# Kernel optimization log

Hardware: AMD Instinct MI355X
Metric: run time of the kernel (lower is better)

## Reference

```python
import jax, jax.numpy as jnp
import numpy as np
from math import sqrt

B, S, D_MODEL = 2, 2048, 1024
H = 16
ADIM = D_MODEL // H  # 64
K_REL = 16
N_PEMB = 2 * K_REL + 1  # 33, bidirectional rel-pos vocabulary


def setup_inputs() -> dict:
    key = jax.random.key(0)
    ks = jax.random.split(key, 8)
    sc = 0.02
    return {
        "iQ": jax.random.normal(ks[0], (B, S, D_MODEL), jnp.float32),
        "iK": jax.random.normal(ks[1], (B, S, D_MODEL), jnp.float32),
        "iV": jax.random.normal(ks[2], (B, S, D_MODEL), jnp.float32),
        "Wq": jax.random.normal(ks[3], (D_MODEL, D_MODEL), jnp.float32) * sc,
        "Wk": jax.random.normal(ks[4], (D_MODEL, D_MODEL), jnp.float32) * sc,
        "Wv": jax.random.normal(ks[5], (D_MODEL, D_MODEL), jnp.float32) * sc,
        "Wo": jax.random.normal(ks[6], (D_MODEL, D_MODEL), jnp.float32) * sc,
        "rel_pemb": jax.random.normal(ks[7], (N_PEMB, ADIM), jnp.float32) * sc,
    }


def reference(iQ, iK, iV, Wq, Wk, Wv, Wo, rel_pemb):
    b, nq, _ = iQ.shape
    seql = iK.shape[1]
    # projections -> [b, h, len, d]
    q = (iQ @ Wq).reshape(b, nq, H, ADIM).transpose(0, 2, 1, 3)
    k = (iK @ Wk).reshape(b, seql, H, ADIM).transpose(0, 2, 1, 3)
    v = (iV @ Wv).reshape(b, seql, H, ADIM).transpose(0, 2, 1, 3)
    # content scores: [b, h, nq, seql]
    scores = jnp.einsum("bhqd,bhsd->bhqs", q, k)
    # relative position bias: rel[i, j] = clamp(j - i, -K, K) + K
    pos = jnp.arange(seql)
    rel = jnp.clip(pos[None, :] - pos[:, None], -K_REL, K_REL) + K_REL
    rel = rel[seql - nq:, :]  # narrow to query rows: [nq, seql]
    e = rel_pemb[rel]  # [nq, seql, d]
    scores = scores + jnp.einsum("bhqd,qsd->bhqs", q, e)
    scores = scores / sqrt(ADIM)
    attn = jax.nn.softmax(scores, axis=-1)
    ctx = jnp.einsum("bhqs,bhsd->bqhd", attn, v).reshape(b, nq, H * ADIM)
    return ctx @ Wo
```

## Files before the change

kernel.cpp:

```cpp
#include <hip/hip_runtime.h>
#include <hip/hip_bf16.h>

#define BB 2
#define S 2048
#define DM 1024
#define H 16
#define ADIM 64
#define NP 33

typedef __bf16 bf16x8 __attribute__((ext_vector_type(8)));
typedef float f32x4 __attribute__((ext_vector_type(4)));

__device__ __forceinline__ void gload16(const void* g, void* l) {
  __builtin_amdgcn_global_load_lds(
      (__attribute__((address_space(1))) void*)(g),
      (__attribute__((address_space(3))) void*)(l), 16, 0, 0);
}

__global__ __launch_bounds__(256) void wtrans(
    const float* __restrict__ W0, const float* __restrict__ W1,
    const float* __restrict__ W2, __bf16* __restrict__ T0,
    __bf16* __restrict__ T1, __bf16* __restrict__ T2) {
  const float* W; __bf16* T;
  switch (blockIdx.z) {
    case 0: W = W0; T = T0; break;
    case 1: W = W1; T = T1; break;
    default: W = W2; T = T2; break;
  }
  __shared__ __bf16 tile[64][65];
  int j = threadIdx.x & 63, i0 = threadIdx.x >> 6;
  int n0 = blockIdx.x * 64, k0 = blockIdx.y * 64;
#pragma unroll
  for (int p = 0; p < 16; ++p) {
    int i = i0 + p * 4;
    tile[i][j] = (__bf16)W[(size_t)(k0 + i) * DM + n0 + j];
  }
  __syncthreads();
#pragma unroll
  for (int p = 0; p < 16; ++p) {
    int i = i0 + p * 4;
    T[(size_t)(n0 + i) * DM + k0 + j] = tile[j][i];
  }
}

#define LDK 40
template <bool A_FP32, typename CT>
__device__ __forceinline__ void gemm_body(const void* __restrict__ Av,
                                          const __bf16* __restrict__ BT,
                                          CT* __restrict__ C, int mode) {
  __shared__ __align__(16) __bf16 As[128 * LDK];
  __shared__ __align__(16) __bf16 Bs[128 * 32];
  int t = threadIdx.x;
  int w = t >> 6, lane = t & 63, l15 = lane & 15, quad = lane >> 4;
  int wm = w >> 1, wn = w & 1;
  int i2 = blockIdx.x + (blockIdx.y << 3);
  int xcd = i2 & 7, slot = i2 >> 3;
  int m0 = (xcd + ((slot >> 3) << 3)) * 128;
  int n0 = (slot & 7) * 128;
  constexpr int LA = A_FP32 ? LDK : 32;
  f32x4 acc[4][4] = {};
  int lr = t >> 2;
  int lk = (t & 3) * 8;
  int r4 = lane >> 2;
  int c8 = (lane & 3) * 8;
  for (int k0 = 0; k0 < DM; k0 += 32) {
    if constexpr (A_FP32) {
#pragma unroll
      for (int rr = 0; rr < 2; ++rr) {
        int row = rr * 64 + lr;
        const float* src = (const float*)Av + (size_t)(m0 + row) * DM + k0 + lk;
        float4 a0 = *(const float4*)src;
        float4 a1 = *(const float4*)(src + 4);
        bf16x8 v;
        v[0] = (__bf16)a0.x; v[1] = (__bf16)a0.y;
        v[2] = (__bf16)a0.z; v[3] = (__bf16)a0.w;
        v[4] = (__bf16)a1.x; v[5] = (__bf16)a1.y;
        v[6] = (__bf16)a1.z; v[7] = (__bf16)a1.w;
        *(bf16x8*)&As[row * LDK + lk] = v;
      }
    } else {
#pragma unroll
      for (int q = 0; q < 2; ++q) {
        int half = w * 2 + q;
        gload16((const __bf16*)Av + (size_t)(m0 + half * 16 + r4) * DM + k0 + c8,
                &As[half * 512]);
      }
    }
#pragma unroll
    for (int q = 0; q < 2; ++q) {
      int half = w * 2 + q;
      gload16(&BT[(size_t)(n0 + half * 16 + r4) * DM + k0 + c8],
              &Bs[half * 512]);
    }
    __syncthreads();
    bf16x8 af[4], bfr[4];
#pragma unroll
    for (int mi = 0; mi < 4; ++mi)
      af[mi] = *(const bf16x8*)&As[(wm * 64 + mi * 16 + l15) * LA + quad * 8];
#pragma unroll
    for (int ni = 0; ni < 4; ++ni)
      bfr[ni] = *(const bf16x8*)&Bs[(wn * 64 + ni * 16 + l15) * 32 + quad * 8];
#pragma unroll
    for (int mi = 0; mi < 4; ++mi)
#pragma unroll
      for (int ni = 0; ni < 4; ++ni)
        acc[mi][ni] = __builtin_amdgcn_mfma_f32_16x16x32_bf16(
            af[mi], bfr[ni], acc[mi][ni], 0, 0, 0);
    __syncthreads();
  }
#pragma unroll
  for (int mi = 0; mi < 4; ++mi)
#pragma unroll
    for (int ni = 0; ni < 4; ++ni)
#pragma unroll
      for (int r = 0; r < 4; ++r) {
        int row = m0 + wm * 64 + mi * 16 + quad * 4 + r;
        int col = n0 + wn * 64 + ni * 16 + l15;
        CT v = (CT)acc[mi][ni][r];
        if (mode == 0) {
          C[(size_t)row * DM + col] = v;
        } else {
          int b = row >> 11, s = row & (S - 1);
          int h = col >> 6, d = col & (ADIM - 1);
          if (mode == 1)
            C[((size_t)(b * H + h) * S + s) * ADIM + d] = v;
          else
            C[((size_t)(b * H + h) * ADIM + d) * S + s] = v;
        }
      }
}

__global__ __launch_bounds__(256) void proj3(
    const float* __restrict__ iQ, const float* __restrict__ iK,
    const float* __restrict__ iV, const __bf16* __restrict__ WqT,
    const __bf16* __restrict__ WkT, const __bf16* __restrict__ WvT,
    __bf16* __restrict__ Qw, __bf16* __restrict__ Kw,
    __bf16* __restrict__ Vt) {
  const float* A; const __bf16* B; __bf16* C; int mode;
  switch (blockIdx.z) {
    case 0: A = iQ; B = WqT; C = Qw; mode = 1; break;
    case 1: A = iK; B = WkT; C = Kw; mode = 1; break;
    default: A = iV; B = WvT; C = Vt; mode = 2; break;
  }
  gemm_body<true, __bf16>(A, B, C, mode);
}

__global__ __launch_bounds__(256) void gemm_final(
    const __bf16* __restrict__ ctx, const __bf16* __restrict__ WoT,
    float* __restrict__ out) {
  gemm_body<false, float>(ctx, WoT, out, 0);
}

#define AST 72
__global__ __launch_bounds__(256) void attn_flash(
    const __bf16* __restrict__ Qw, const __bf16* __restrict__ Kw,
    const __bf16* __restrict__ Vt, const float* __restrict__ pemb,
    __bf16* __restrict__ ctx) {
  int bh = blockIdx.y, b = bh >> 4, h = bh & 15;
  int q0 = blockIdx.x * 64;
  int t = threadIdx.x, w = t >> 6, lane = t & 63, l15 = lane & 15,
      quad = lane >> 4;
  const __bf16* Qh = Qw + (size_t)bh * S * ADIM;
  const __bf16* Kh = Kw + (size_t)bh * S * ADIM;
  const __bf16* Vh = Vt + (size_t)bh * ADIM * S;

  __shared__ __align__(16) char smem[36352];
  __bf16* Ks = (__bf16*)smem;
  __bf16* Vs = (__bf16*)(smem + 9216);
  float* pband = (float*)(smem + 18432);
  __bf16* pbufw = (__bf16*)(smem + 27136 + w * 2304);
  __bf16* peb = (__bf16*)smem;

  for (int i = t; i < 48 * 64; i += 256) {
    int r = i >> 6, d = i & 63;
    peb[r * AST + d] = (r < NP) ? (__bf16)pemb[i] : (__bf16)0.f;
  }

  int qa = q0 + w * 16 + l15;
  bf16x8 qf0 = *(const bf16x8*)&Qh[(size_t)qa * ADIM + quad * 8];
  bf16x8 qf1 = *(const bf16x8*)&Qh[(size_t)qa * ADIM + 32 + quad * 8];
  __syncthreads();

  {
    f32x4 pc[3] = {};
#pragma unroll
    for (int ni = 0; ni < 3; ++ni) {
      bf16x8 b0 = *(const bf16x8*)&peb[(ni * 16 + l15) * AST + quad * 8];
      bf16x8 b1 = *(const bf16x8*)&peb[(ni * 16 + l15) * AST + 32 + quad * 8];
      pc[ni] = __builtin_amdgcn_mfma_f32_16x16x32_bf16(qf0, b0, pc[ni], 0, 0, 0);
      pc[ni] = __builtin_amdgcn_mfma_f32_16x16x32_bf16(qf1, b1, pc[ni], 0, 0, 0);
    }
#pragma unroll
    for (int ni = 0; ni < 3; ++ni)
#pragma unroll
      for (int r = 0; r < 4; ++r) {
        int col = ni * 16 + l15;
        if (col < NP) pband[(w * 16 + quad * 4 + r) * 34 + col] = pc[ni][r];
      }
  }
  __syncthreads();

  int qc = q0 + w * 16 + quad * 4;
  int lrow = w * 16 + quad * 4;
  int qw0 = q0 + w * 16;
  float lsum[4] = {0.f, 0.f, 0.f, 0.f};
  f32x4 o[4] = {};

  float blo[4], bhi[4];
#pragma unroll
  for (int r = 0; r < 4; ++r) {
    blo[r] = __expf(pband[(lrow + r) * 34 + 0] * 0.125f);
    bhi[r] = __expf(pband[(lrow + r) * 34 + 32] * 0.125f);
  }

  int srow = t >> 3;
  int scol = (t & 7) * 8;
  bf16x8 k0r = *(const bf16x8*)&Kh[(size_t)srow * ADIM + scol];
  bf16x8 k1r = *(const bf16x8*)&Kh[(size_t)(32 + srow) * ADIM + scol];
  bf16x8 v0r = *(const bf16x8*)&Vh[(size_t)srow * S + scol];
  bf16x8 v1r = *(const bf16x8*)&Vh[(size_t)(32 + srow) * S + scol];

  for (int s0 = 0; s0 < S; s0 += 64) {
    __syncthreads();
    *(bf16x8*)&Ks[srow * AST + scol] = k0r;
    *(bf16x8*)&Ks[(32 + srow) * AST + scol] = k1r;
    *(bf16x8*)&Vs[srow * AST + scol] = v0r;
    *(bf16x8*)&Vs[(32 + srow) * AST + scol] = v1r;
    int sn = s0 + 64;
    if (sn < S) {
      k0r = *(const bf16x8*)&Kh[(size_t)(sn + srow) * ADIM + scol];
      k1r = *(const bf16x8*)&Kh[(size_t)(sn + 32 + srow) * ADIM + scol];
      v0r = *(const bf16x8*)&Vh[(size_t)srow * S + sn + scol];
      v1r = *(const bf16x8*)&Vh[(size_t)(32 + srow) * S + sn + scol];
    }
    __syncthreads();

    f32x4 c[4];
#pragma unroll
    for (int j = 0; j < 4; ++j) {
      f32x4 cj = {};
      bf16x8 kb0 = *(const bf16x8*)&Ks[(j * 16 + l15) * AST + quad * 8];
      bf16x8 kb1 = *(const bf16x8*)&Ks[(j * 16 + l15) * AST + 32 + quad * 8];
      cj = __builtin_amdgcn_mfma_f32_16x16x32_bf16(qf0, kb0, cj, 0, 0, 0);
      cj = __builtin_amdgcn_mfma_f32_16x16x32_bf16(qf1, kb1, cj, 0, 0, 0);
      c[j] = cj;
    }

    float pv[4][4];
    bool below = (s0 + 79 <= qw0);
    bool above = (s0 >= qw0 + 31);
    if (below || above) {
#pragma unroll
      for (int j = 0; j < 4; ++j)
#pragma unroll
        for (int r = 0; r < 4; ++r) {
          float f = below ? blo[r] : bhi[r];
          float e = __expf(c[j][r] * 0.125f) * f;
          lsum[r] += e;
          pv[j][r] = e;
        }
    } else {
#pragma unroll
      for (int j = 0; j < 4; ++j)
#pragma unroll
        for (int r = 0; r < 4; ++r) {
          int qg = qc + r;
          int sg = s0 + j * 16 + l15;
          int i0 = sg - qg; i0 = i0 < -16 ? -16 : (i0 > 16 ? 16 : i0); i0 += 16;
          float e = __expf((c[j][r] + pband[(lrow + r) * 34 + i0]) * 0.125f);
          lsum[r] += e;
          pv[j][r] = e;
        }
    }

#pragma unroll
    for (int j = 0; j < 4; ++j)
#pragma unroll
      for (int r = 0; r < 4; ++r)
        pbufw[(quad * 4 + r) * AST + j * 16 + l15] = (__bf16)pv[j][r];
    bf16x8 pa0 = *(const bf16x8*)&pbufw[l15 * AST + quad * 8];
    bf16x8 pa1 = *(const bf16x8*)&pbufw[l15 * AST + 32 + quad * 8];

#pragma unroll
    for (int nt = 0; nt < 4; ++nt) {
      bf16x8 vb0 = *(const bf16x8*)&Vs[(nt * 16 + l15) * AST + quad * 8];
      bf16x8 vb1 = *(const bf16x8*)&Vs[(nt * 16 + l15) * AST + 32 + quad * 8];
      o[nt] = __builtin_amdgcn_mfma_f32_16x16x32_bf16(pa0, vb0, o[nt], 0, 0, 0);
      o[nt] = __builtin_amdgcn_mfma_f32_16x16x32_bf16(pa1, vb1, o[nt], 0, 0, 0);
    }
  }

#pragma unroll
  for (int r = 0; r < 4; ++r) {
#pragma unroll
    for (int mm = 1; mm < 16; mm <<= 1) lsum[r] += __shfl_xor(lsum[r], mm, 64);
  }
#pragma unroll
  for (int nt = 0; nt < 4; ++nt)
#pragma unroll
    for (int r = 0; r < 4; ++r) {
      int qg = qc + r;
      int d = nt * 16 + l15;
      ctx[(size_t)(b * S + qg) * DM + h * ADIM + d] =
          (__bf16)(o[nt][r] / lsum[r]);
    }
}

extern "C" void kernel_launch(void* const* d_in, const int* in_sizes, int n_in,
                              void* d_out, int out_size, void* d_ws,
                              size_t ws_size, hipStream_t stream) {
  bool sizes_ok =
      (n_in == 8 && in_sizes[0] == BB * S * DM && in_sizes[1] == BB * S * DM &&
       in_sizes[2] == BB * S * DM && in_sizes[3] == DM * DM &&
       in_sizes[4] == DM * DM && in_sizes[5] == DM * DM &&
       in_sizes[6] == DM * DM && in_sizes[7] == NP * ADIM &&
       out_size == BB * S * DM);
  if (!sizes_ok) return;
  if (ws_size < 33ull * 1024 * 1024) return;

  const float* iQ = (const float*)d_in[0];
  const float* iK = (const float*)d_in[1];
  const float* iV = (const float*)d_in[2];
  const float* Wq = (const float*)d_in[3];
  const float* Wk = (const float*)d_in[4];
  const float* Wv = (const float*)d_in[5];
  const float* Wo = (const float*)d_in[6];
  const float* pemb = (const float*)d_in[7];

  char* w = (char*)d_ws;
  const size_t MB = 1024 * 1024;
  __bf16* Qw  = (__bf16*)(w + 0 * MB);
  __bf16* Kw  = (__bf16*)(w + 8 * MB);
  __bf16* Vt  = (__bf16*)(w + 16 * MB);
  __bf16* ctx = (__bf16*)(w + 24 * MB);
  __bf16* WqT = (__bf16*)(w + 24 * MB);
  __bf16* WkT = (__bf16*)(w + 26 * MB);
  __bf16* WvT = (__bf16*)(w + 28 * MB);
  __bf16* WoT = (__bf16*)(w + 0 * MB);

  wtrans<<<dim3(16, 16, 3), 256, 0, stream>>>(Wq, Wk, Wv, WqT, WkT, WvT);
  proj3<<<dim3(8, 32, 3), 256, 0, stream>>>(iQ, iK, iV, WqT, WkT, WvT,
                                            Qw, Kw, Vt);
  attn_flash<<<dim3(S / 64, BB * H), 256, 0, stream>>>(Qw, Kw, Vt, pemb, ctx);
  wtrans<<<dim3(16, 16, 1), 256, 0, stream>>>(Wo, Wo, Wo, WoT, WoT, WoT);
  gemm_final<<<dim3(8, 32), 256, 0, stream>>>(ctx, WoT, (float*)d_out);
}
```

Baseline: 266.9 us.

## Pre-convert inputs to bf16, narrow final GEMM tiles, remap attention blocks, use exp2

Adds a separate kernel that converts the fp32 Q/K/V inputs to bf16, so the projection GEMM can stream its A operand with async global-to-LDS loads instead of converting in registers. It runs only when the workspace is large enough. The output GEMM now uses 128x64 tiles, which doubles the block count, and gets an XCD-aware block mapping. Attention blocks are remapped across XCDs, and the softmax exponent uses exp2 with a folded log2e scale so the positional bias can be absorbed into an FMA. The cost is an extra kernel launch plus an additional round trip of the inputs through memory.

```diff
diff --git a/kernel.cpp b/kernel.cpp
--- a/kernel.cpp
+++ b/kernel.cpp
@@ -15,6 +15,27 @@
   __builtin_amdgcn_global_load_lds(
       (__attribute__((address_space(1))) void*)(g),
       (__attribute__((address_space(3))) void*)(l), 16, 0, 0);
+}
+
+__global__ __launch_bounds__(256) void tobf16(
+    const float* __restrict__ X0, const float* __restrict__ X1,
+    const float* __restrict__ X2, __bf16* __restrict__ Y0,
+    __bf16* __restrict__ Y1, __bf16* __restrict__ Y2) {
+  const float* X; __bf16* Y;
+  switch (blockIdx.z) {
+    case 0: X = X0; Y = Y0; break;
+    case 1: X = X1; Y = Y1; break;
+    default: X = X2; Y = Y2; break;
+  }
+  size_t i = ((size_t)blockIdx.x * 256 + threadIdx.x) * 8;
+  float4 a0 = *(const float4*)(X + i);
+  float4 a1 = *(const float4*)(X + i + 4);
+  bf16x8 v;
+  v[0] = (__bf16)a0.x; v[1] = (__bf16)a0.y;
+  v[2] = (__bf16)a0.z; v[3] = (__bf16)a0.w;
+  v[4] = (__bf16)a1.x; v[5] = (__bf16)a1.y;
+  v[6] = (__bf16)a1.z; v[7] = (__bf16)a1.w;
+  *(bf16x8*)(Y + i) = v;
 }
 
 __global__ __launch_bounds__(256) void wtrans(
@@ -44,21 +65,20 @@
 }
 
 #define LDK 40
-template <bool A_FP32, typename CT>
+template <bool A_FP32, int BN, typename CT>
 __device__ __forceinline__ void gemm_body(const void* __restrict__ Av,
                                           const __bf16* __restrict__ BT,
-                                          CT* __restrict__ C, int mode) {
+                                          CT* __restrict__ C, int mode,
+                                          int m0, int n0) {
+  constexpr int NF = BN / 32;
+  constexpr int BH = BN / 16;
   __shared__ __align__(16) __bf16 As[128 * LDK];
-  __shared__ __align__(16) __bf16 Bs[128 * 32];
+  __shared__ __align__(16) __bf16 Bs[BN * 32];
   int t = threadIdx.x;
   int w = t >> 6, lane = t & 63, l15 = lane & 15, quad = lane >> 4;
   int wm = w >> 1, wn = w & 1;
-  int i2 = blockIdx.x + (blockIdx.y << 3);
-  int xcd = i2 & 7, slot = i2 >> 3;
-  int m0 = (xcd + ((slot >> 3) << 3)) * 128;
-  int n0 = (slot & 7) * 128;
   constexpr int LA = A_FP32 ? LDK : 32;
-  f32x4 acc[4][4] = {};
+  f32x4 acc[4][NF] = {};
   int lr = t >> 2;
   int lk = (t & 3) * 8;
   int r4 = lane >> 2;
@@ -87,23 +107,24 @@
       }
     }
 #pragma unroll
-    for (int q = 0; q < 2; ++q) {
-      int half = w * 2 + q;
+    for (int q = 0; q < BH / 4; ++q) {
+      int half = w * (BH / 4) + q;
       gload16(&BT[(size_t)(n0 + half * 16 + r4) * DM + k0 + c8],
               &Bs[half * 512]);
     }
     __syncthreads();
-    bf16x8 af[4], bfr[4];
+    bf16x8 af[4], bfr[NF];
 #pragma unroll
     for (int mi = 0; mi < 4; ++mi)
       af[mi] = *(const bf16x8*)&As[(wm * 64 + mi * 16 + l15) * LA + quad * 8];
 #pragma unroll
-    for (int ni = 0; ni < 4; ++ni)
-      bfr[ni] = *(const bf16x8*)&Bs[(wn * 64 + ni * 16 + l15) * 32 + quad * 8];
+    for (int ni = 0; ni < NF; ++ni)
+      bfr[ni] =
+          *(const bf16x8*)&Bs[(wn * (BN / 2) + ni * 16 + l15) * 32 + quad * 8];
 #pragma unroll
     for (int mi = 0; mi < 4; ++mi)
 #pragma unroll
-      for (int ni = 0; ni < 4; ++ni)
+      for (int ni = 0; ni < NF; ++ni)
         acc[mi][ni] = __builtin_amdgcn_mfma_f32_16x16x32_bf16(
             af[mi], bfr[ni], acc[mi][ni], 0, 0, 0);
     __syncthreads();
@@ -111,11 +132,11 @@
 #pragma unroll
   for (int mi = 0; mi < 4; ++mi)
 #pragma unroll
-    for (int ni = 0; ni < 4; ++ni)
+    for (int ni = 0; ni < NF; ++ni)
 #pragma unroll
       for (int r = 0; r < 4; ++r) {
         int row = m0 + wm * 64 + mi * 16 + quad * 4 + r;
-        int col = n0 + wn * 64 + ni * 16 + l15;
+        int col = n0 + wn * (BN / 2) + ni * 16 + l15;
         CT v = (CT)acc[mi][ni][r];
         if (mode == 0) {
           C[(size_t)row * DM + col] = v;
@@ -142,13 +163,40 @@
     case 1: A = iK; B = WkT; C = Kw; mode = 1; break;
     default: A = iV; B = WvT; C = Vt; mode = 2; break;
   }
-  gemm_body<true, __bf16>(A, B, C, mode);
+  int i2 = blockIdx.x + (blockIdx.y << 3);
+  int xcd = i2 & 7, slot = i2 >> 3;
+  int m0 = (xcd + ((slot >> 3) << 3)) * 128;
+  int n0 = (slot & 7) * 128;
+  gemm_body<true, 128, __bf16>(A, B, C, mode, m0, n0);
+}
+
+__global__ __launch_bounds__(256) void proj3b(
+    const __bf16* __restrict__ Qb, const __bf16* __restrict__ Kb,
+    const __bf16* __restrict__ Vb, const __bf16* __restrict__ WqT,
+    const __bf16* __restrict__ WkT, const __bf16* __restrict__ WvT,
+    __bf16* __restrict__ Qw, __bf16* __restrict__ Kw,
+    __bf16* __restrict__ Vt) {
+  const __bf16* A; const __bf16* B; __bf16* C; int mode;
+  switch (blockIdx.z) {
+    case 0: A = Qb; B = WqT; C = Qw; mode = 1; break;
+    case 1: A = Kb; B = WkT; C = Kw; mode = 1; break;
+    default: A = Vb; B = WvT; C = Vt; mode = 2; break;
+  }
+  int i2 = blockIdx.x + (blockIdx.y << 3);
+  int xcd = i2 & 7, slot = i2 >> 3;
+  int m0 = (xcd + ((slot >> 3) << 3)) * 128;
+  int n0 = (slot & 7) * 128;
+  gemm_body<false, 128, __bf16>(A, B, C, mode, m0, n0);
 }
 
 __global__ __launch_bounds__(256) void gemm_final(
     const __bf16* __restrict__ ctx, const __bf16* __restrict__ WoT,
     float* __restrict__ out) {
-  gemm_body<false, float>(ctx, WoT, out, 0);
+  int i2 = blockIdx.x + (blockIdx.y << 4);
+  int xcd = i2 & 7, slot = i2 >> 3;
+  int m0 = ((xcd << 2) + (slot >> 4)) * 128;
+  int n0 = (slot & 15) * 64;
+  gemm_body<false, 64, float>(ctx, WoT, out, 0, m0, n0);
 }
 
 #define AST 72
@@ -156,8 +204,11 @@
     const __bf16* __restrict__ Qw, const __bf16* __restrict__ Kw,
     const __bf16* __restrict__ Vt, const float* __restrict__ pemb,
     __bf16* __restrict__ ctx) {
-  int bh = blockIdx.y, b = bh >> 4, h = bh & 15;
-  int q0 = blockIdx.x * 64;
+  int i = blockIdx.x + (blockIdx.y << 5);
+  int a = i & 7, m = i >> 3;
+  int bh = m >> 2;
+  int q0 = ((a << 2) + (m & 3)) * 64;
+  int b = bh >> 4, h = bh & 15;
   int t = threadIdx.x, w = t >> 6, lane = t & 63, l15 = lane & 15,
       quad = lane >> 4;
   const __bf16* Qh = Qw + (size_t)bh * S * ADIM;
@@ -171,9 +222,9 @@
   __bf16* pbufw = (__bf16*)(smem + 27136 + w * 2304);
   __bf16* peb = (__bf16*)smem;
 
-  for (int i = t; i < 48 * 64; i += 256) {
-    int r = i >> 6, d = i & 63;
-    peb[r * AST + d] = (r < NP) ? (__bf16)pemb[i] : (__bf16)0.f;
+  for (int ii = t; ii < 48 * 64; ii += 256) {
+    int r = ii >> 6, d = ii & 63;
+    peb[r * AST + d] = (r < NP) ? (__bf16)pemb[ii] : (__bf16)0.f;
   }
 
   int qa = q0 + w * 16 + l15;
@@ -206,11 +257,12 @@
   float lsum[4] = {0.f, 0.f, 0.f, 0.f};
   f32x4 o[4] = {};
 
-  float blo[4], bhi[4];
+  const float K2 = 0.18033688011112f;
+  float pK0[4], pK32[4];
 #pragma unroll
   for (int r = 0; r < 4; ++r) {
-    blo[r] = __expf(pband[(lrow + r) * 34 + 0] * 0.125f);
-    bhi[r] = __expf(pband[(lrow + r) * 34 + 32] * 0.125f);
+    pK0[r] = pband[(lrow + r) * 34 + 0] * K2;
+    pK32[r] = pband[(lrow + r) * 34 + 32] * K2;
   }
 
   int srow = t >> 3;
@@ -254,8 +306,8 @@
       for (int j = 0; j < 4; ++j)
 #pragma unroll
         for (int r = 0; r < 4; ++r) {
-          float f = below ? blo[r] : bhi[r];
-          float e = __expf(c[j][r] * 0.125f) * f;
+          float pk = below ? pK0[r] : pK32[r];
+          float e = exp2f(__builtin_fmaf(c[j][r], K2, pk));
           lsum[r] += e;
           pv[j][r] = e;
         }
@@ -267,7 +319,7 @@
           int qg = qc + r;
           int sg = s0 + j * 16 + l15;
           int i0 = sg - qg; i0 = i0 < -16 ? -16 : (i0 > 16 ? 16 : i0); i0 += 16;
-          float e = __expf((c[j][r] + pband[(lrow + r) * 34 + i0]) * 0.125f);
+          float e = exp2f((c[j][r] + pband[(lrow + r) * 34 + i0]) * K2);
           lsum[r] += e;
           pv[j][r] = e;
         }
@@ -339,9 +391,18 @@
   __bf16* WoT = (__bf16*)(w + 0 * MB);
 
   wtrans<<<dim3(16, 16, 3), 256, 0, stream>>>(Wq, Wk, Wv, WqT, WkT, WvT);
-  proj3<<<dim3(8, 32, 3), 256, 0, stream>>>(iQ, iK, iV, WqT, WkT, WvT,
-                                            Qw, Kw, Vt);
+  if (ws_size >= 56ull * 1024 * 1024) {
+    __bf16* Qb = (__bf16*)(w + 32 * MB);
+    __bf16* Kb = (__bf16*)(w + 40 * MB);
+    __bf16* Vb = (__bf16*)(w + 48 * MB);
+    tobf16<<<dim3(2048, 1, 3), 256, 0, stream>>>(iQ, iK, iV, Qb, Kb, Vb);
+    proj3b<<<dim3(8, 32, 3), 256, 0, stream>>>(Qb, Kb, Vb, WqT, WkT, WvT,
+                                               Qw, Kw, Vt);
+  } else {
+    proj3<<<dim3(8, 32, 3), 256, 0, stream>>>(iQ, iK, iV, WqT, WkT, WvT,
+                                              Qw, Kw, Vt);
+  }
   attn_flash<<<dim3(S / 64, BB * H), 256, 0, stream>>>(Qw, Kw, Vt, pemb, ctx);
   wtrans<<<dim3(16, 16, 1), 256, 0, stream>>>(Wo, Wo, Wo, WoT, WoT, WoT);
-  gemm_final<<<dim3(8, 32), 256, 0, stream>>>(ctx, WoT, (float*)d_out);
-}
+  gemm_final<<<dim3(16, 32), 256, 0, stream>>>(ctx, WoT, (float*)d_out);
+}
```

Measured after the change: 257.4 us. 3.5% less time.
